# Kernel tuning notes

Hardware: AMD Instinct MI355X
Metric: run time of the kernel (lower is better)

## Reference

```python
import jax, jax.numpy as jnp
import numpy as np

D = 20          # embedding dim (hardcoded in original module)
N_REL = 200     # relation vocab size (table has N_REL+1 rows)
N_TIME = 365    # time embedding table size
L = 3           # propagation layers
E = 2_000_000   # edges per layer
N = 1_000_000   # node-slot pool per layer
B = 64          # batch size
N_ENT = 1_000_003


def setup_inputs() -> dict:
    key = jax.random.key(0)
    ks = jax.random.split(key, 16)
    src_idx = jax.random.randint(ks[0], (L, E), 0, N, dtype=jnp.int32)
    dst_idx = jax.random.randint(ks[1], (L, E), 0, N, dtype=jnp.int32)
    rel_idx = jax.random.randint(ks[2], (L, E), 0, N_REL + 1, dtype=jnp.int32)
    qrel_idx = jax.random.randint(ks[3], (L, E), 0, N_REL + 1, dtype=jnp.int32)
    # signed relative time (edge_time - query_time); abs() must stay < N_TIME
    rel_time = jax.random.randint(ks[4], (L, E), -(N_TIME - 1), N_TIME, dtype=jnp.int32)
    node_batch = jax.random.randint(ks[5], (N,), 0, B, dtype=jnp.int32)
    node_ent = jnp.arange(N, dtype=jnp.int32)  # unique entity per final node slot
    s = 0.1
    rela_embed = jax.random.normal(ks[6], (N_REL + 1, D), jnp.float32) * s
    time_embed = jax.random.normal(ks[7], (N_TIME, D), jnp.float32) * s
    w_att1 = jax.random.normal(ks[8], (30, 3 * D), jnp.float32) * s
    w_att2 = jax.random.normal(ks[9], (1, 30), jnp.float32) * s
    w_past = jax.random.normal(ks[10], (D, D), jnp.float32) * s
    w_now = jax.random.normal(ks[11], (D, D), jnp.float32) * s
    w_future = jax.random.normal(ks[12], (D, D), jnp.float32) * s
    w_cls = jax.random.normal(ks[13], (D,), jnp.float32) * s
    b_cls = jnp.zeros((), jnp.float32)
    return dict(src_idx=src_idx, dst_idx=dst_idx, rel_idx=rel_idx,
                qrel_idx=qrel_idx, rel_time=rel_time, node_batch=node_batch,
                node_ent=node_ent, rela_embed=rela_embed, time_embed=time_embed,
                w_att1=w_att1, w_att2=w_att2, w_past=w_past, w_now=w_now,
                w_future=w_future, w_cls=w_cls, b_cls=b_cls,
                batch_size=B, n_ent=N_ENT)


def reference(src_idx, dst_idx, rel_idx, qrel_idx, rel_time, node_batch,
              node_ent, rela_embed, time_embed, w_att1, w_att2, w_past,
              w_now, w_future, w_cls, b_cls, batch_size, n_ent):
    n_layers = src_idx.shape[0]
    n_nodes = node_batch.shape[0]
    d = rela_embed.shape[1]
    hidden = jnp.zeros((n_nodes, d), dtype=rela_embed.dtype)
    for l in range(n_layers):
        rt = rel_time[l]                         # [E] signed relative time
        h_src = hidden[src_idx[l]]               # [E, D] gather
        r_emb = rela_embed[rel_idx[l]]           # [E, D]
        t_emb = time_embed[jnp.abs(rt)]          # [E, D]
        embed_rel = h_src + r_emb + t_emb
        # conditional time-branch MLP (mask-partitioned linear, same math as
        # the original's boolean-masked assignments)
        fut = embed_rel @ w_future.T
        now = embed_rel @ w_now.T
        pst = embed_rel @ w_past.T
        transformed = jnp.where((rt > 0)[:, None], fut,
                       jnp.where((rt == 0)[:, None], now, pst))
        # attention over concat(hidden_src, rel_emb, query_rel_emb)  [E, 3D]
        att_in = jnp.concatenate([h_src, r_emb, rela_embed[qrel_idx[l]]], axis=1)
        score = jax.nn.sigmoid(jax.nn.relu(att_in @ w_att1.T) @ w_att2.T)  # [E,1]
        msg = score * transformed                # [E, D]
        hidden = jax.ops.segment_sum(msg, dst_idx[l], num_segments=n_nodes)
        hidden = jax.nn.leaky_relu(hidden)       # default slope 0.01, as torch
    result = hidden @ w_cls + b_cls              # [N]
    score_all = jnp.zeros((batch_size, n_ent), dtype=result.dtype)
    score_all = score_all.at[node_batch, node_ent].set(result)
    return score_all
```

## Files before the change

kernel.cpp:

```cpp
#include <hip/hip_runtime.h>
#include <hip/hip_bf16.h>
#include <cstdint>

#define DD 20
#define HID 30
#define NB_SCAN 1024
#define HROW 32

typedef unsigned int  u32;
typedef unsigned short u16;

__device__ __forceinline__ void load20(const float* __restrict__ p, float* r){
  const float4* q = (const float4*)p;
#pragma unroll
  for (int i=0;i<5;i++){ float4 v=q[i]; r[4*i+0]=v.x; r[4*i+1]=v.y; r[4*i+2]=v.z; r[4*i+3]=v.w; }
}

__device__ __forceinline__ u32 pkbf(float a, float b){
  u32 ua=__float_as_uint(a); ua=(ua+0x7FFFu+((ua>>16)&1u))>>16;
  u32 ub=__float_as_uint(b); ub=(ub+0x7FFFu+((ub>>16)&1u))>>16;
  return ua | (ub<<16);
}

__global__ void k_prep(const float* __restrict__ rela, const float* __restrict__ w1,
                       const float* __restrict__ wp, const float* __restrict__ wn,
                       const float* __restrict__ wf,
                       float* __restrict__ W3, float* __restrict__ AR, float* __restrict__ AQ,
                       int nrel){
  int t = blockIdx.x*blockDim.x + threadIdx.x;
  if (t < 3*DD*DD){
    int s = t/(DD*DD), idx = t%(DD*DD);
    W3[t] = (s==0)?wp[idx]:((s==1)?wn[idx]:wf[idx]);
  }
  if (t < nrel*HID){
    int r=t/HID, j=t-r*HID;
    float sr=0.f, sq=0.f;
#pragma unroll
    for (int k=0;k<DD;k++){
      float e = rela[r*DD+k];
      sr += e*w1[j*3*DD + DD + k];
      sq += e*w1[j*3*DD + 2*DD + k];
    }
    AR[r*32+j]=sr; AQ[r*32+j]=sq;
  }
}

__global__ void k_rwtw(const float* __restrict__ rela, const float* __restrict__ timee,
                       const float* __restrict__ W3,
                       float* __restrict__ RW, float* __restrict__ TW,
                       int nrel, int ntime){
  int t = blockIdx.x*blockDim.x+threadIdx.x;
  int totR = 3*nrel*DD, totT = 3*ntime*DD;
  if (t < totR){
    int sel = t/(nrel*DD); int rem = t - sel*nrel*DD; int r = rem/DD; int i = rem - r*DD;
    const float* w = W3 + sel*DD*DD + i*DD;
    const float* e = rela + (size_t)r*DD;
    float s=0.f;
#pragma unroll
    for (int k=0;k<DD;k++) s += e[k]*w[k];
    RW[t]=s;
  }
  if (t < totT){
    int sel = t/(ntime*DD); int rem = t - sel*ntime*DD; int tt = rem/DD; int i = rem - tt*DD;
    const float* w = W3 + sel*DD*DD + i*DD;
    const float* e = timee + (size_t)tt*DD;
    float s=0.f;
#pragma unroll
    for (int k=0;k<DD;k++) s += e[k]*w[k];
    TW[t]=s;
  }
}

__global__ void k_rt(const float* __restrict__ rela, const float* __restrict__ timee,
                     const float* __restrict__ W3, float* __restrict__ RT,
                     int nrel, int ntime){
  int row = blockIdx.x*blockDim.x+threadIdx.x;
  int tot = 3*nrel*ntime;
  if (row>=tot) return;
  int per = nrel*ntime;
  int sel = row/per; int rem = row - sel*per; int r = rem/ntime; int t = rem - r*ntime;
  float e[DD], tv[DD];
  load20(rela + (size_t)r*DD, e);
  load20(timee + (size_t)t*DD, tv);
#pragma unroll
  for (int k=0;k<DD;k++) e[k]+=tv[k];
  const float* W = W3 + sel*DD*DD;
  float o[DD];
#pragma unroll
  for (int i=0;i<DD;i++){
    const float4* wr = (const float4*)(W + i*DD);
    float s=0.f;
#pragma unroll
    for (int c=0;c<5;c++){ float4 w=wr[c]; s += e[4*c]*w.x + e[4*c+1]*w.y + e[4*c+2]*w.z + e[4*c+3]*w.w; }
    o[i]=s;
  }
  float4* op=(float4*)(RT + (size_t)row*DD);
#pragma unroll
  for (int c=0;c<5;c++){ float4 v; v.x=o[4*c]; v.y=o[4*c+1]; v.z=o[4*c+2]; v.w=o[4*c+3]; op[c]=v; }
}

__global__ void __launch_bounds__(256) k_pre(const int* __restrict__ dst, int* __restrict__ cnt,
        int* __restrict__ rank, int E, int N,
        float4* __restrict__ dout4, size_t nd4,
        uint4* __restrict__ b0, uint4* __restrict__ b1, size_t nbB4,
        float4* __restrict__ bF, size_t nf4,
        float4* __restrict__ res4, size_t nr4){
  int g=blockIdx.x, tid=threadIdx.x;
  int half=gridDim.x>>1;
  if (g & 1){
    int stride=half*256;
    int E2=2*E;
    for (int e=(g>>1)*256+tid; e<E2; e+=stride){
      int l=(e>=E)?1:0;
      rank[e]=atomicAdd(&cnt[(size_t)l*N+dst[e]],1);
    }
  } else {
    float4 z=make_float4(0.f,0.f,0.f,0.f);
    uint4 zu=make_uint4(0u,0u,0u,0u);
    size_t i=(size_t)(g>>1)*256+tid, st=(size_t)half*256;
    for (size_t k=i;k<nd4;k+=st) dout4[k]=z;
    for (size_t k=i;k<nbB4;k+=st){ b0[k]=zu; b1[k]=zu; }
    for (size_t k=i;k<nf4;k+=st) bF[k]=z;
    for (size_t k=i;k<nr4;k+=st) res4[k]=z;
  }
}

__global__ void k_scan_part(const int* __restrict__ cnt, int* __restrict__ part, int M, int C){
  __shared__ int sm[256];
  int b=blockIdx.x, t=threadIdx.x;
  int lo=b*C, hi=lo+C; if (hi>M) hi=M; if (lo>M) lo=M;
  int s=0;
  for (int i=lo+t; i<hi; i+=256) s+=cnt[i];
  sm[t]=s; __syncthreads();
  for (int o=128;o>0;o>>=1){ if (t<o) sm[t]+=sm[t+o]; __syncthreads(); }
  if (t==0) part[b]=sm[0];
}

__global__ void k_scan_top(int* __restrict__ part, int* __restrict__ listc){
  __shared__ int sm[NB_SCAN];
  int t=threadIdx.x;
  if (t==0) *listc=0;
  int v=part[t]; sm[t]=v; __syncthreads();
  for (int o=1;o<NB_SCAN;o<<=1){
    int u=(t>=o)?sm[t-o]:0; __syncthreads();
    sm[t]+=u; __syncthreads();
  }
  part[t]=sm[t]-v;
}

__global__ void k_scan_write(const int* __restrict__ cnt, const int* __restrict__ part,
                             int* __restrict__ rowptr, int M, int C){
  __shared__ int sm[256];
  int b=blockIdx.x, t=threadIdx.x;
  int lo=b*C, hi=lo+C; if (hi>M) hi=M; if (lo>M) lo=M;
  int run=part[b];
  for (int base=lo; base<hi; base+=256){
    int i=base+t;
    int v=(i<hi)?cnt[i]:0;
    sm[t]=v; __syncthreads();
    for (int o=1;o<256;o<<=1){
      int u=(t>=o)?sm[t-o]:0; __syncthreads();
      sm[t]+=u; __syncthreads();
    }
    if (i<hi) rowptr[i]=run+sm[t]-v;
    int tot=sm[255];
    __syncthreads();
    run+=tot;
  }
  if (hi==M && t==0) rowptr[M]=run;
}

__global__ void __launch_bounds__(256) k_scat(const int* __restrict__ src,const int* __restrict__ dst,
  const int* __restrict__ rel,const int* __restrict__ qrel,const int* __restrict__ rtm,
  const int* __restrict__ rank,const int* __restrict__ rowptr,int4* __restrict__ recs,int E){
  int e=blockIdx.x*blockDim.x+threadIdx.x;
  if (e>=E) return;
  int d=dst[e];
  int pos=rowptr[d]+rank[e];
  recs[pos]=make_int4(src[e], rel[e]|(qrel[e]<<16), rtm[e], d);
}

template<bool HASH,bool FINAL,int XR>
__global__ void __launch_bounds__(256) k_fused(
    const int4* __restrict__ recs,
    const u16* __restrict__ hin, u16* __restrict__ hout, float* __restrict__ bufF,
    const float* __restrict__ RW, const float* __restrict__ TW,
    const float* __restrict__ AR, const float* __restrict__ AQ,
    const float* __restrict__ w1, const float* __restrict__ w2, const float* __restrict__ W3,
    int E, int nrel, int ntime,
    const int* __restrict__ sA_src, const int* __restrict__ sA_dst,
    const int* __restrict__ sA_rel, const int* __restrict__ sA_qrel,
    const int* __restrict__ sA_rtm, const int* __restrict__ sA_rank,
    const int* __restrict__ sA_rowptr, int4* __restrict__ sA_recs, int sA_E,
    const int* __restrict__ hB_dst, int* __restrict__ hB_cnt, int* __restrict__ hB_rank, int hB_E,
    const float* __restrict__ wcls, float* __restrict__ res,
    int* __restrict__ list, int* __restrict__ listc)
{
  int g=blockIdx.x;
  if (XR>0){
    const int M=2+XR;
    int r=g%M, b=g/M, R=gridDim.x/M;
    if (r==2){
      int stride=R*256;
      for (int e=b*256+threadIdx.x; e<sA_E; e+=stride){
        int d=sA_dst[e];
        int pos=sA_rowptr[d]+sA_rank[e];
        sA_recs[pos]=make_int4(sA_src[e], sA_rel[e]|(sA_qrel[e]<<16), sA_rtm[e], d);
      }
      return;
    }
    if (XR>1 && r==3){
      int stride=R*256;
      for (int e=b*256+threadIdx.x; e<hB_E; e+=stride)
        hB_rank[e]=atomicAdd(&hB_cnt[hB_dst[e]],1);
      return;
    }
    g = b*2+r;
  }
  int bstart=g*256;
  if (bstart>=E) return;

  __shared__ float sW1h[HID*DD];
  __shared__ float sW2[32];
  __shared__ float sW3[3*DD*DD];
  __shared__ u32   smsg[256*10];
  __shared__ int   sdst[256];
  __shared__ int   s_prevdst, s_nextdst;
  if (HASH){
    for (int t=threadIdx.x; t<HID*DD; t+=blockDim.x){ int j=t/DD,k=t-j*DD; sW1h[t]=w1[j*3*DD+k]; }
    for (int t=threadIdx.x; t<3*DD*DD; t+=blockDim.x) sW3[t]=W3[t];
  }
  if (threadIdx.x<HID) sW2[threadIdx.x]=w2[threadIdx.x];

  int tid = threadIdx.x;
  int bsize = E - bstart; if (bsize>256) bsize=256;
  int j = bstart + tid;
  bool active = (tid < bsize);

  if (tid==0){
    s_prevdst = (bstart>0) ? recs[-1 + (ptrdiff_t)bstart].w : -1;
    s_nextdst = (bstart+bsize < E) ? recs[bstart+bsize].w : -1;
  }
  __syncthreads();

  int dstv = -1;
  float m[DD];
  if (active){
    int4 rc = recs[j];
    int s = rc.x;
    int r = rc.y & 0xFFFF;
    int q = ((unsigned)rc.y) >> 16;
    int t = rc.z;
    dstv  = rc.w;
    int sel = (t>0)?2:((t==0)?1:0);
    int ta = (t<0)?-t:t;

    float h[DD];
    if (HASH){
      const uint4* hp=(const uint4*)(hin+(size_t)s*HROW);
      uint4 A=hp[0], B=hp[1]; uint2 Cc=*((const uint2*)(hp+2));
      h[0]=__uint_as_float(A.x<<16);  h[1]=__uint_as_float(A.x&0xFFFF0000u);
      h[2]=__uint_as_float(A.y<<16);  h[3]=__uint_as_float(A.y&0xFFFF0000u);
      h[4]=__uint_as_float(A.z<<16);  h[5]=__uint_as_float(A.z&0xFFFF0000u);
      h[6]=__uint_as_float(A.w<<16);  h[7]=__uint_as_float(A.w&0xFFFF0000u);
      h[8]=__uint_as_float(B.x<<16);  h[9]=__uint_as_float(B.x&0xFFFF0000u);
      h[10]=__uint_as_float(B.y<<16); h[11]=__uint_as_float(B.y&0xFFFF0000u);
      h[12]=__uint_as_float(B.z<<16); h[13]=__uint_as_float(B.z&0xFFFF0000u);
      h[14]=__uint_as_float(B.w<<16); h[15]=__uint_as_float(B.w&0xFFFF0000u);
      h[16]=__uint_as_float(Cc.x<<16);h[17]=__uint_as_float(Cc.x&0xFFFF0000u);
      h[18]=__uint_as_float(Cc.y<<16);h[19]=__uint_as_float(Cc.y&0xFFFF0000u);
    }

    float z=0.f;
    {
      const float4* ap=(const float4*)(AR+(size_t)r*32);
      const float4* qp=(const float4*)(AQ+(size_t)q*32);
#pragma unroll
      for (int c=0;c<7;c++){
        float4 x=ap[c], y=qp[c];
        float s4[4]={x.x+y.x, x.y+y.y, x.z+y.z, x.w+y.w};
#pragma unroll
        for (int u=0;u<4;u++){
          int jj=4*c+u;
          if (HASH){
            const float4* wr=(const float4*)&sW1h[jj*DD];
            float sum=s4[u];
#pragma unroll
            for (int c2=0;c2<5;c2++){ float4 w=wr[c2]; sum += h[4*c2]*w.x+h[4*c2+1]*w.y+h[4*c2+2]*w.z+h[4*c2+3]*w.w; }
            s4[u]=sum;
          }
          z += fmaxf(s4[u],0.f)*sW2[jj];
        }
      }
      float2 x2=*(const float2*)(AR+(size_t)r*32+28);
      float2 y2=*(const float2*)(AQ+(size_t)q*32+28);
      float s0=x2.x+y2.x, s1=x2.y+y2.y;
      if (HASH){
        const float4* wr0=(const float4*)&sW1h[28*DD];
        const float4* wr1=(const float4*)&sW1h[29*DD];
#pragma unroll
        for (int c2=0;c2<5;c2++){
          float4 wA=wr0[c2], wB=wr1[c2];
          s0 += h[4*c2]*wA.x+h[4*c2+1]*wA.y+h[4*c2+2]*wA.z+h[4*c2+3]*wA.w;
          s1 += h[4*c2]*wB.x+h[4*c2+1]*wB.y+h[4*c2+2]*wB.z+h[4*c2+3]*wB.w;
        }
      }
      z += fmaxf(s0,0.f)*sW2[28] + fmaxf(s1,0.f)*sW2[29];
    }
    float score = 1.f/(1.f+__expf(-z));

    const float4* rwp=(const float4*)(RW + ((size_t)(sel*nrel+r))*DD);
    const float4* twp=(const float4*)(TW + ((size_t)(sel*ntime+ta))*DD);
#pragma unroll
    for (int c=0;c<5;c++){
      float4 a4=rwp[c], b4=twp[c];
      float mv[4]={a4.x+b4.x, a4.y+b4.y, a4.z+b4.z, a4.w+b4.w};
      if (HASH){
#pragma unroll
        for (int u=0;u<4;u++){
          const float4* wr=(const float4*)&sW3[sel*DD*DD+(4*c+u)*DD];
          float sum=mv[u];
#pragma unroll
          for (int c2=0;c2<5;c2++){ float4 w=wr[c2]; sum += h[4*c2]*w.x+h[4*c2+1]*w.y+h[4*c2+2]*w.z+h[4*c2+3]*w.w; }
          mv[u]=sum;
        }
      }
#pragma unroll
      for (int u=0;u<4;u++) m[4*c+u]=score*mv[u];
    }
#pragma unroll
    for (int i2=0;i2<10;i2++) smsg[tid*10+i2]=pkbf(m[2*i2],m[2*i2+1]);
  }
  sdst[tid] = active ? dstv : -2;
  __syncthreads();

  if (!active) return;
  bool isHead = (tid==0) ? (s_prevdst != dstv) : (sdst[tid-1] != dstv);
  if (!(isHead || tid==0)) return;
  int k=tid+1;
  for (; k<bsize && sdst[k]==dstv; ++k){
    const u32* row=&smsg[k*10];
#pragma unroll
    for (int i2=0;i2<10;i2++){
      u32 w=row[i2];
      m[2*i2]  +=__uint_as_float(w<<16);
      m[2*i2+1]+=__uint_as_float(w&0xFFFF0000u);
    }
  }
  bool crossStart = (tid==0 && !isHead);
  bool crossEnd   = (k==bsize) && (s_nextdst==dstv);
  if (crossStart || crossEnd){
    float* o = bufF + (size_t)dstv*DD;
#pragma unroll
    for (int i=0;i<DD;i++) atomicAdd(o+i, m[i]);
    if (!FINAL && isHead){
      int p = atomicAdd(listc,1);
      list[p] = dstv;
    }
  } else {
    if (!FINAL){
      u32 o10[10];
#pragma unroll
      for (int i2=0;i2<10;i2++){
        float x0=m[2*i2], x1=m[2*i2+1];
        x0=fmaxf(x0,0.01f*x0); x1=fmaxf(x1,0.01f*x1);
        o10[i2]=pkbf(x0,x1);
      }
      uint4* hp=(uint4*)(hout+(size_t)dstv*HROW);
      hp[0]=make_uint4(o10[0],o10[1],o10[2],o10[3]);
      hp[1]=make_uint4(o10[4],o10[5],o10[6],o10[7]);
      *((uint2*)(hp+2))=make_uint2(o10[8],o10[9]);
    } else {
      float rsum=0.f;
#pragma unroll
      for (int i=0;i<DD;i++){ float x=fmaxf(m[i],0.01f*m[i]); rsum += x*wcls[i]; }
      res[dstv] = rsum;
    }
  }
}

__global__ void __launch_bounds__(256) k_fixup(float* __restrict__ bufF, u16* __restrict__ hout,
   const int* __restrict__ list,const int* __restrict__ listc){
  int c=*listc;
  for (int i=blockIdx.x*blockDim.x+threadIdx.x; i<c; i+=gridDim.x*blockDim.x){
    int n=list[i];
    float* p=bufF+(size_t)n*DD;
    float v[DD];
#pragma unroll
    for (int jj=0;jj<DD;jj++){ v[jj]=p[jj]; p[jj]=0.f; }
    u32 o10[10];
#pragma unroll
    for (int i2=0;i2<10;i2++){
      float x0=v[2*i2], x1=v[2*i2+1];
      x0=fmaxf(x0,0.01f*x0); x1=fmaxf(x1,0.01f*x1);
      o10[i2]=pkbf(x0,x1);
    }
    uint4* hp=(uint4*)(hout+(size_t)n*HROW);
    hp[0]=make_uint4(o10[0],o10[1],o10[2],o10[3]);
    hp[1]=make_uint4(o10[4],o10[5],o10[6],o10[7]);
    *((uint2*)(hp+2))=make_uint2(o10[8],o10[9]);
  }
}

__global__ void __launch_bounds__(256) k_out(const float* __restrict__ res,
   const float* __restrict__ bufF, const float* __restrict__ wcls, const float* __restrict__ bcls,
   const int* __restrict__ nb, const int* __restrict__ ne, const int* __restrict__ nentp,
   float* __restrict__ out, int N){
  int n=blockIdx.x*blockDim.x+threadIdx.x;
  if (n>=N) return;
  float acc = res[n] + bcls[0];
  const float4* q=(const float4*)(bufF+(size_t)n*DD);
#pragma unroll
  for (int c=0;c<5;c++){
    float4 v=q[c];
    acc += fmaxf(v.x,0.01f*v.x)*wcls[4*c]   + fmaxf(v.y,0.01f*v.y)*wcls[4*c+1]
         + fmaxf(v.z,0.01f*v.z)*wcls[4*c+2] + fmaxf(v.w,0.01f*v.w)*wcls[4*c+3];
  }
  long long stride = nentp[0];
  out[(long long)nb[n]*stride + ne[n]] = acc;
}

template<bool HASH>
__global__ void __launch_bounds__(256) k_edge(
    const int* __restrict__ src, const int* __restrict__ dst,
    const int* __restrict__ rel, const int* __restrict__ qrel,
    const int* __restrict__ rtm,
    const float* __restrict__ hin, float* __restrict__ hout,
    const float* __restrict__ RT, const float* __restrict__ AR, const float* __restrict__ AQ,
    const float* __restrict__ w1, const float* __restrict__ w2, const float* __restrict__ W3,
    int E, int nrel, int ntime)
{
  __shared__ float sW1h[HID*DD];
  __shared__ float sW2[32];
  __shared__ float sW3[3*DD*DD];
  for (int t=threadIdx.x; t<HID*DD; t+=blockDim.x){ int j=t/DD,k=t-j*DD; sW1h[t]=w1[j*3*DD+k]; }
  if (threadIdx.x<HID) sW2[threadIdx.x]=w2[threadIdx.x];
  for (int t=threadIdx.x; t<3*DD*DD; t+=blockDim.x) sW3[t]=W3[t];
  __syncthreads();
  int e = blockIdx.x*blockDim.x+threadIdx.x;
  if (e>=E) return;
  int s=src[e], d=dst[e], r=rel[e], q=qrel[e], t=rtm[e];
  int sel = (t>0)?2:((t==0)?1:0);
  int ta = (t<0)?-t:t;
  float h[DD];
  if (HASH){
    load20(hin+(size_t)s*DD, h);
#pragma unroll
    for (int i=0;i<DD;i++) h[i]=fmaxf(h[i],0.01f*h[i]);
  }
  float a[HID];
  {
    const float4* ap=(const float4*)(AR+(size_t)r*32);
    const float4* qp=(const float4*)(AQ+(size_t)q*32);
#pragma unroll
    for (int c=0;c<7;c++){
      float4 x=ap[c], y=qp[c];
      a[4*c+0]=x.x+y.x; a[4*c+1]=x.y+y.y; a[4*c+2]=x.z+y.z; a[4*c+3]=x.w+y.w;
    }
    float2 x=*(const float2*)(AR+(size_t)r*32+28);
    float2 y=*(const float2*)(AQ+(size_t)q*32+28);
    a[28]=x.x+y.x; a[29]=x.y+y.y;
  }
  if (HASH){
#pragma unroll
    for (int j=0;j<HID;j++){
      const float4* wr=(const float4*)&sW1h[j*DD];
      float sum=a[j];
#pragma unroll
      for (int c=0;c<5;c++){ float4 w=wr[c]; sum += h[4*c]*w.x+h[4*c+1]*w.y+h[4*c+2]*w.z+h[4*c+3]*w.w; }
      a[j]=sum;
    }
  }
  float z=0.f;
#pragma unroll
  for (int j=0;j<HID;j++) z += fmaxf(a[j],0.f)*sW2[j];
  float score = 1.f/(1.f+__expf(-z));
  float tr[DD];
  load20(RT + ((size_t)(sel*nrel+r)*ntime + ta)*DD, tr);
  if (HASH){
    const float* Ws = sW3 + sel*DD*DD;
#pragma unroll
    for (int i=0;i<DD;i++){
      const float4* wr=(const float4*)(Ws+i*DD);
      float sum=tr[i];
#pragma unroll
      for (int c=0;c<5;c++){ float4 w=wr[c]; sum += h[4*c]*w.x+h[4*c+1]*w.y+h[4*c+2]*w.z+h[4*c+3]*w.w; }
      tr[i]=sum;
    }
  }
  float* o = hout + (size_t)d*DD;
#pragma unroll
  for (int i=0;i<DD;i++) atomicAdd(o+i, score*tr[i]);
}

__global__ void k_result(const float* __restrict__ h, const float* __restrict__ wcls,
                         const float* __restrict__ bcls, float* __restrict__ res, int N){
  int i = blockIdx.x*blockDim.x+threadIdx.x;
  if (i>=N) return;
  float acc = bcls[0];
  const float4* q=(const float4*)(h+(size_t)i*DD);
#pragma unroll
  for (int c=0;c<5;c++){
    float4 v=q[c];
    float x0=fmaxf(v.x,0.01f*v.x), x1=fmaxf(v.y,0.01f*v.y);
    float x2=fmaxf(v.z,0.01f*v.z), x3=fmaxf(v.w,0.01f*v.w);
    acc += x0*wcls[4*c]+x1*wcls[4*c+1]+x2*wcls[4*c+2]+x3*wcls[4*c+3];
  }
  res[i]=acc;
}

__global__ void k_scatter(const float* __restrict__ res, const int* __restrict__ nb,
                          const int* __restrict__ ne, const int* __restrict__ nentp,
                          float* __restrict__ out, int N){
  int i=blockIdx.x*blockDim.x+threadIdx.x;
  if (i>=N) return;
  long long stride = nentp[0];
  out[(long long)nb[i]*stride + ne[i]] = res[i];
}

extern "C" void kernel_launch(void* const* d_in, const int* in_sizes, int n_in,
                              void* d_out, int out_size, void* d_ws, size_t ws_size,
                              hipStream_t stream){
  const int*   src =(const int*)d_in[0];
  const int*   dst =(const int*)d_in[1];
  const int*   rel =(const int*)d_in[2];
  const int*   qrel=(const int*)d_in[3];
  const int*   rtm =(const int*)d_in[4];
  const int*   nb  =(const int*)d_in[5];
  const int*   ne  =(const int*)d_in[6];
  const float* rela=(const float*)d_in[7];
  const float* timee=(const float*)d_in[8];
  const float* w1  =(const float*)d_in[9];
  const float* w2  =(const float*)d_in[10];
  const float* wp  =(const float*)d_in[11];
  const float* wn  =(const float*)d_in[12];
  const float* wf  =(const float*)d_in[13];
  const float* wcls=(const float*)d_in[14];
  const float* bcls=(const float*)d_in[15];
  const int*   nentp=(const int*)d_in[17];

  const int Lc=3;
  int LE=in_sizes[0]; int E=LE/Lc;
  int N=in_sizes[5];
  int nrel=in_sizes[7]/DD;
  int ntime=in_sizes[8]/DD;

  auto al=[](size_t x){ return (x+(size_t)255)&~(size_t)255; };
  size_t szBufB=al((size_t)N*HROW*2);
  size_t szBufF=al((size_t)N*DD*4);
  size_t szBuf =al((size_t)N*DD*4);
  size_t szRW  =al((size_t)3*nrel*DD*4);
  size_t szTW  =al((size_t)3*ntime*DD*4);
  size_t szRTf =al((size_t)3*nrel*ntime*DD*4);
  size_t szA   =al((size_t)nrel*32*4);
  size_t szW3  =al((size_t)3*DD*DD*4);
  size_t szRow =al((size_t)Lc*((size_t)N+1)*4);
  size_t szRank=al((size_t)LE*4);
  size_t szCnt =al((size_t)Lc*N*4);
  size_t szRecs=al((size_t)LE*16);
  size_t szPart=al((size_t)NB_SCAN*4);
  size_t szList=al((size_t)(131072+16)*4);
  size_t szRes =al((size_t)N*4);
  size_t need = 2*szBufB+szBufF+szRW+szTW+2*szA+szW3+szRow+szRank+szCnt+szRecs+szPart+szList+szRes;

  dim3 blk(256);
  int prepTot = (3*DD*DD > nrel*HID) ? 3*DD*DD : nrel*HID;
  int rtTot=3*nrel*ntime;
  int rwtwTot = 3*ntime*DD;

  if (ws_size >= need){
    char* base=(char*)d_ws;
    size_t off=0;
    u16*   b0 =(u16*)(base+off);   off+=szBufB;
    u16*   b1 =(u16*)(base+off);   off+=szBufB;
    float* bufF=(float*)(base+off); off+=szBufF;
    float* RW  =(float*)(base+off); off+=szRW;
    float* TW  =(float*)(base+off); off+=szTW;
    float* AR  =(float*)(base+off); off+=szA;
    float* AQ  =(float*)(base+off); off+=szA;
    float* W3  =(float*)(base+off); off+=szW3;
    int*   rowptr=(int*)(base+off); off+=szRow;
    int*   rank=(int*)(base+off);  off+=szRank;
    int*   cnt =(int*)(base+off);  off+=szCnt;
    int4*  recs=(int4*)(base+off); off+=szRecs;
    int*   part=(int*)(base+off);  off+=szPart;
    int*   listc=(int*)(base+off);
    int*   list =listc+16;          off+=szList;
    float* res =(float*)(base+off); off+=szRes;

    float* dout=(float*)d_out;

    (void)hipMemsetAsync(cnt,0,(size_t)Lc*N*4,stream);
    k_prep<<<dim3((prepTot+255)/256),blk,0,stream>>>(rela,w1,wp,wn,wf,W3,AR,AQ,nrel);
    k_rwtw<<<dim3((rwtwTot+255)/256),blk,0,stream>>>(rela,timee,W3,RW,TW,nrel,ntime);

    size_t nd4=(size_t)out_size>>2;
    size_t nbB4=(size_t)N*HROW*2/16;
    size_t nf4=(size_t)N*DD/4;
    size_t nr4=(size_t)N/4;
    k_pre<<<dim3(8192),blk,0,stream>>>(dst,cnt,rank,E,N,(float4*)dout,nd4,
                                       (uint4*)b0,(uint4*)b1,nbB4,(float4*)bufF,nf4,
                                       (float4*)res,nr4);

    int C=(N+NB_SCAN-1)/NB_SCAN;
    int LB=(E+255)/256;
    int H=(LB+1)/2;

    for (int l=0;l<2;++l){
      int* cnt_l = cnt + (size_t)l*N;
      int* row_l = rowptr + (size_t)l*(N+1);
      k_scan_part<<<dim3(NB_SCAN),blk,0,stream>>>(cnt_l,part,N,C);
      k_scan_top<<<dim3(1),dim3(NB_SCAN),0,stream>>>(part,listc);
      k_scan_write<<<dim3(NB_SCAN),blk,0,stream>>>(cnt_l,part,row_l,N,C);
    }
    k_scat<<<dim3(LB),blk,0,stream>>>(src,dst,rel,qrel,rtm,rank,rowptr,recs,E);

    k_fused<false,false,2><<<dim3(4*H),blk,0,stream>>>(recs,nullptr,b0,bufF,
        RW,TW,AR,AQ,w1,w2,W3,E,nrel,ntime,
        src+(size_t)E,dst+(size_t)E,rel+(size_t)E,qrel+(size_t)E,rtm+(size_t)E,
        rank+(size_t)E,rowptr+(size_t)(N+1),recs+(size_t)E,E,
        dst+(size_t)2*E,cnt+(size_t)2*N,rank+(size_t)2*E,E,
        wcls,res,list,listc);
    k_fixup<<<dim3(128),blk,0,stream>>>(bufF,b0,list,listc);

    {
      int* cnt_l = cnt + (size_t)2*N;
      int* row_l = rowptr + (size_t)2*(N+1);
      k_scan_part<<<dim3(NB_SCAN),blk,0,stream>>>(cnt_l,part,N,C);
      k_scan_top<<<dim3(1),dim3(NB_SCAN),0,stream>>>(part,listc);
      k_scan_write<<<dim3(NB_SCAN),blk,0,stream>>>(cnt_l,part,row_l,N,C);
    }

    k_fused<true,false,1><<<dim3(3*H),blk,0,stream>>>(recs+(size_t)E,b0,b1,bufF,
        RW,TW,AR,AQ,w1,w2,W3,E,nrel,ntime,
        src+(size_t)2*E,dst+(size_t)2*E,rel+(size_t)2*E,qrel+(size_t)2*E,rtm+(size_t)2*E,
        rank+(size_t)2*E,rowptr+(size_t)2*(N+1),recs+(size_t)2*E,E,
        nullptr,nullptr,nullptr,0,
        wcls,res,list,listc);
    k_fixup<<<dim3(128),blk,0,stream>>>(bufF,b1,list,listc);

    k_fused<true,true,0><<<dim3(LB),blk,0,stream>>>(recs+(size_t)2*E,b1,nullptr,bufF,
        RW,TW,AR,AQ,w1,w2,W3,E,nrel,ntime,
        nullptr,nullptr,nullptr,nullptr,nullptr,nullptr,nullptr,nullptr,0,
        nullptr,nullptr,nullptr,0,
        wcls,res,list,listc);

    k_out<<<dim3((N+255)/256),blk,0,stream>>>(res,bufF,wcls,bcls,nb,ne,nentp,dout,N);
  } else {
    char* base=(char*)d_out; float* res=(float*)d_ws;
    size_t off=0;
    float* buf0=(float*)(base+off); off+=szBuf;
    float* buf1=(float*)(base+off); off+=szBuf;
    float* RT  =(float*)(base+off); off+=szRTf;
    float* AR  =(float*)(base+off); off+=szA;
    float* AQ  =(float*)(base+off); off+=szA;
    float* W3  =(float*)(base+off); off+=szW3;
    k_prep<<<dim3((prepTot+255)/256),blk,0,stream>>>(rela,w1,wp,wn,wf,W3,AR,AQ,nrel);
    k_rt<<<dim3((rtTot+255)/256),blk,0,stream>>>(rela,timee,W3,RT,nrel,ntime);
    dim3 egrid((E+255)/256);
    dim3 ngrid((N+255)/256);
    (void)hipMemsetAsync(buf0,0,(size_t)N*DD*4,stream);
    k_edge<false><<<egrid,blk,0,stream>>>(src,dst,rel,qrel,rtm,nullptr,buf0,RT,AR,AQ,w1,w2,W3,E,nrel,ntime);
    (void)hipMemsetAsync(buf1,0,(size_t)N*DD*4,stream);
    k_edge<true><<<egrid,blk,0,stream>>>(src+(size_t)E,dst+(size_t)E,rel+(size_t)E,qrel+(size_t)E,rtm+(size_t)E,
                                         buf0,buf1,RT,AR,AQ,w1,w2,W3,E,nrel,ntime);
    (void)hipMemsetAsync(buf0,0,(size_t)N*DD*4,stream);
    k_edge<true><<<egrid,blk,0,stream>>>(src+(size_t)2*E,dst+(size_t)2*E,rel+(size_t)2*E,qrel+(size_t)2*E,rtm+(size_t)2*E,
                                         buf1,buf0,RT,AR,AQ,w1,w2,W3,E,nrel,ntime);
    k_result<<<ngrid,blk,0,stream>>>(buf0,wcls,bcls,res,N);
    (void)hipMemsetAsync(d_out,0,(size_t)out_size*sizeof(float),stream);
    k_scatter<<<ngrid,blk,0,stream>>>(res,nb,ne,nentp,(float*)d_out,N);
  }
}
```

Baseline: 1.102 ms.

## Store hidden states in fp32 and merge layer 0/1 scans and scatters

Replaces the bf16 packed hidden-state buffers (32-element padded rows) with plain fp32 20-float rows. Leaky ReLU now runs on the consumer side, and shared-memory message staging uses fp32 with a padded row stride of 21. The layer-0 and layer-1 prefix scans and record scatters are merged into one scan over 2N counts and one scatter kernel. Layer-2's scatter moves out of the fused layer-1 kernel into its own launch. This cuts launch count and pack/unpack ALU work, but each hidden-state gather row grows from 64 to 80 bytes and the shared-memory footprint rises.

Measured after the change: 1.053 ms. -4.4%, faster.

```diff
diff --git a/kernel.cpp b/kernel.cpp
--- a/kernel.cpp
+++ b/kernel.cpp
@@ -5,7 +5,7 @@
 #define DD 20
 #define HID 30
 #define NB_SCAN 1024
-#define HROW 32
+#define MROW 21
 
 typedef unsigned int  u32;
 typedef unsigned short u16;
@@ -14,12 +14,6 @@
   const float4* q = (const float4*)p;
 #pragma unroll
   for (int i=0;i<5;i++){ float4 v=q[i]; r[4*i+0]=v.x; r[4*i+1]=v.y; r[4*i+2]=v.z; r[4*i+3]=v.w; }
-}
-
-__device__ __forceinline__ u32 pkbf(float a, float b){
-  u32 ua=__float_as_uint(a); ua=(ua+0x7FFFu+((ua>>16)&1u))>>16;
-  u32 ub=__float_as_uint(b); ub=(ub+0x7FFFu+((ub>>16)&1u))>>16;
-  return ua | (ub<<16);
 }
 
 __global__ void k_prep(const float* __restrict__ rela, const float* __restrict__ w1,
@@ -102,7 +96,7 @@
 __global__ void __launch_bounds__(256) k_pre(const int* __restrict__ dst, int* __restrict__ cnt,
         int* __restrict__ rank, int E, int N,
         float4* __restrict__ dout4, size_t nd4,
-        uint4* __restrict__ b0, uint4* __restrict__ b1, size_t nbB4,
+        float4* __restrict__ b0, float4* __restrict__ b1, size_t nb4,
         float4* __restrict__ bF, size_t nf4,
         float4* __restrict__ res4, size_t nr4){
   int g=blockIdx.x, tid=threadIdx.x;
@@ -116,10 +110,9 @@
     }
   } else {
     float4 z=make_float4(0.f,0.f,0.f,0.f);
-    uint4 zu=make_uint4(0u,0u,0u,0u);
     size_t i=(size_t)(g>>1)*256+tid, st=(size_t)half*256;
     for (size_t k=i;k<nd4;k+=st) dout4[k]=z;
-    for (size_t k=i;k<nbB4;k+=st){ b0[k]=zu; b1[k]=zu; }
+    for (size_t k=i;k<nb4;k+=st){ b0[k]=z; b1[k]=z; }
     for (size_t k=i;k<nf4;k+=st) bF[k]=z;
     for (size_t k=i;k<nr4;k+=st) res4[k]=z;
   }
@@ -149,13 +142,13 @@
 }
 
 __global__ void k_scan_write(const int* __restrict__ cnt, const int* __restrict__ part,
-                             int* __restrict__ rowptr, int M, int C){
+                             int* __restrict__ rowptr, int M, int C, int base){
   __shared__ int sm[256];
   int b=blockIdx.x, t=threadIdx.x;
   int lo=b*C, hi=lo+C; if (hi>M) hi=M; if (lo>M) lo=M;
-  int run=part[b];
-  for (int base=lo; base<hi; base+=256){
-    int i=base+t;
+  int run=part[b]+base;
+  for (int bb=lo; bb<hi; bb+=256){
+    int i=bb+t;
     int v=(i<hi)?cnt[i]:0;
     sm[t]=v; __syncthreads();
     for (int o=1;o<256;o<<=1){
@@ -170,60 +163,59 @@
   if (hi==M && t==0) rowptr[M]=run;
 }
 
-__global__ void __launch_bounds__(256) k_scat(const int* __restrict__ src,const int* __restrict__ dst,
+__global__ void __launch_bounds__(256) k_scat01(const int* __restrict__ src,const int* __restrict__ dst,
   const int* __restrict__ rel,const int* __restrict__ qrel,const int* __restrict__ rtm,
-  const int* __restrict__ rank,const int* __restrict__ rowptr,int4* __restrict__ recs,int E){
+  const int* __restrict__ rank,const int* __restrict__ rowptr,int4* __restrict__ recs,int E,int N){
+  int e=blockIdx.x*blockDim.x+threadIdx.x;
+  if (e>=2*E) return;
+  int l=(e>=E)?1:0;
+  int d=dst[e];
+  int pos=rowptr[(size_t)l*N+d]+rank[e];
+  recs[pos]=make_int4(src[e], rel[e]|(qrel[e]<<16), rtm[e], d);
+}
+
+__global__ void __launch_bounds__(256) k_scat2(const int* __restrict__ src,const int* __restrict__ dst,
+  const int* __restrict__ rel,const int* __restrict__ qrel,const int* __restrict__ rtm,
+  const int* __restrict__ rank,const int* __restrict__ rowptr2,int4* __restrict__ recs,int E){
   int e=blockIdx.x*blockDim.x+threadIdx.x;
   if (e>=E) return;
   int d=dst[e];
-  int pos=rowptr[d]+rank[e];
+  int pos=rowptr2[d]+rank[e];
   recs[pos]=make_int4(src[e], rel[e]|(qrel[e]<<16), rtm[e], d);
 }
 
-template<bool HASH,bool FINAL,int XR>
+template<bool HASH,bool FINAL,bool HIST>
 __global__ void __launch_bounds__(256) k_fused(
     const int4* __restrict__ recs,
-    const u16* __restrict__ hin, u16* __restrict__ hout, float* __restrict__ bufF,
+    const float* __restrict__ hin, float* __restrict__ hout, float* __restrict__ bufF,
     const float* __restrict__ RW, const float* __restrict__ TW,
     const float* __restrict__ AR, const float* __restrict__ AQ,
     const float* __restrict__ w1, const float* __restrict__ w2, const float* __restrict__ W3,
     int E, int nrel, int ntime,
-    const int* __restrict__ sA_src, const int* __restrict__ sA_dst,
-    const int* __restrict__ sA_rel, const int* __restrict__ sA_qrel,
-    const int* __restrict__ sA_rtm, const int* __restrict__ sA_rank,
-    const int* __restrict__ sA_rowptr, int4* __restrict__ sA_recs, int sA_E,
     const int* __restrict__ hB_dst, int* __restrict__ hB_cnt, int* __restrict__ hB_rank, int hB_E,
     const float* __restrict__ wcls, float* __restrict__ res,
     int* __restrict__ list, int* __restrict__ listc)
 {
-  int g=blockIdx.x;
-  if (XR>0){
-    const int M=2+XR;
-    int r=g%M, b=g/M, R=gridDim.x/M;
-    if (r==2){
-      int stride=R*256;
-      for (int e=b*256+threadIdx.x; e<sA_E; e+=stride){
-        int d=sA_dst[e];
-        int pos=sA_rowptr[d]+sA_rank[e];
-        sA_recs[pos]=make_int4(sA_src[e], sA_rel[e]|(sA_qrel[e]<<16), sA_rtm[e], d);
-      }
-      return;
-    }
-    if (XR>1 && r==3){
-      int stride=R*256;
-      for (int e=b*256+threadIdx.x; e<hB_E; e+=stride)
+  int lb;
+  if (HIST){
+    int g=blockIdx.x;
+    int r3=g%3, b3=g/3;
+    if (r3==2){
+      int H=gridDim.x/3;
+      int stride=H*256;
+      for (int e=b3*256+threadIdx.x; e<hB_E; e+=stride)
         hB_rank[e]=atomicAdd(&hB_cnt[hB_dst[e]],1);
       return;
     }
-    g = b*2+r;
-  }
-  int bstart=g*256;
+    lb=b3*2+r3;
+  } else lb=blockIdx.x;
+  int bstart=lb*256;
   if (bstart>=E) return;
 
   __shared__ float sW1h[HID*DD];
   __shared__ float sW2[32];
   __shared__ float sW3[3*DD*DD];
-  __shared__ u32   smsg[256*10];
+  __shared__ float smsg[256*MROW];
   __shared__ int   sdst[256];
   __shared__ int   s_prevdst, s_nextdst;
   if (HASH){
@@ -257,18 +249,9 @@
 
     float h[DD];
     if (HASH){
-      const uint4* hp=(const uint4*)(hin+(size_t)s*HROW);
-      uint4 A=hp[0], B=hp[1]; uint2 Cc=*((const uint2*)(hp+2));
-      h[0]=__uint_as_float(A.x<<16);  h[1]=__uint_as_float(A.x&0xFFFF0000u);
-      h[2]=__uint_as_float(A.y<<16);  h[3]=__uint_as_float(A.y&0xFFFF0000u);
-      h[4]=__uint_as_float(A.z<<16);  h[5]=__uint_as_float(A.z&0xFFFF0000u);
-      h[6]=__uint_as_float(A.w<<16);  h[7]=__uint_as_float(A.w&0xFFFF0000u);
-      h[8]=__uint_as_float(B.x<<16);  h[9]=__uint_as_float(B.x&0xFFFF0000u);
-      h[10]=__uint_as_float(B.y<<16); h[11]=__uint_as_float(B.y&0xFFFF0000u);
-      h[12]=__uint_as_float(B.z<<16); h[13]=__uint_as_float(B.z&0xFFFF0000u);
-      h[14]=__uint_as_float(B.w<<16); h[15]=__uint_as_float(B.w&0xFFFF0000u);
-      h[16]=__uint_as_float(Cc.x<<16);h[17]=__uint_as_float(Cc.x&0xFFFF0000u);
-      h[18]=__uint_as_float(Cc.y<<16);h[19]=__uint_as_float(Cc.y&0xFFFF0000u);
+      load20(hin+(size_t)s*DD, h);
+#pragma unroll
+      for (int i=0;i<DD;i++) h[i]=fmaxf(h[i],0.01f*h[i]);
     }
 
     float z=0.f;
@@ -326,10 +309,8 @@
         }
       }
 #pragma unroll
-      for (int u=0;u<4;u++) m[4*c+u]=score*mv[u];
-    }
-#pragma unroll
-    for (int i2=0;i2<10;i2++) smsg[tid*10+i2]=pkbf(m[2*i2],m[2*i2+1]);
+      for (int u=0;u<4;u++){ m[4*c+u]=score*mv[u]; smsg[tid*MROW+4*c+u]=m[4*c+u]; }
+    }
   }
   sdst[tid] = active ? dstv : -2;
   __syncthreads();
@@ -339,13 +320,9 @@
   if (!(isHead || tid==0)) return;
   int k=tid+1;
   for (; k<bsize && sdst[k]==dstv; ++k){
-    const u32* row=&smsg[k*10];
-#pragma unroll
-    for (int i2=0;i2<10;i2++){
-      u32 w=row[i2];
-      m[2*i2]  +=__uint_as_float(w<<16);
-      m[2*i2+1]+=__uint_as_float(w&0xFFFF0000u);
-    }
+    const float* row=&smsg[k*MROW];
+#pragma unroll
+    for (int i=0;i<DD;i++) m[i]+=row[i];
   }
   bool crossStart = (tid==0 && !isHead);
   bool crossEnd   = (k==bsize) && (s_nextdst==dstv);
@@ -359,17 +336,9 @@
     }
   } else {
     if (!FINAL){
-      u32 o10[10];
-#pragma unroll
-      for (int i2=0;i2<10;i2++){
-        float x0=m[2*i2], x1=m[2*i2+1];
-        x0=fmaxf(x0,0.01f*x0); x1=fmaxf(x1,0.01f*x1);
-        o10[i2]=pkbf(x0,x1);
-      }
-      uint4* hp=(uint4*)(hout+(size_t)dstv*HROW);
-      hp[0]=make_uint4(o10[0],o10[1],o10[2],o10[3]);
-      hp[1]=make_uint4(o10[4],o10[5],o10[6],o10[7]);
-      *((uint2*)(hp+2))=make_uint2(o10[8],o10[9]);
+      float4* op=(float4*)(hout + (size_t)dstv*DD);
+#pragma unroll
+      for (int c=0;c<5;c++){ float4 v; v.x=m[4*c]; v.y=m[4*c+1]; v.z=m[4*c+2]; v.w=m[4*c+3]; op[c]=v; }
     } else {
       float rsum=0.f;
 #pragma unroll
@@ -379,26 +348,15 @@
   }
 }
 
-__global__ void __launch_bounds__(256) k_fixup(float* __restrict__ bufF, u16* __restrict__ hout,
+__global__ void __launch_bounds__(256) k_fixup(float* __restrict__ bufF, float* __restrict__ hout,
    const int* __restrict__ list,const int* __restrict__ listc){
   int c=*listc;
   for (int i=blockIdx.x*blockDim.x+threadIdx.x; i<c; i+=gridDim.x*blockDim.x){
     int n=list[i];
     float* p=bufF+(size_t)n*DD;
-    float v[DD];
-#pragma unroll
-    for (int jj=0;jj<DD;jj++){ v[jj]=p[jj]; p[jj]=0.f; }
-    u32 o10[10];
-#pragma unroll
-    for (int i2=0;i2<10;i2++){
-      float x0=v[2*i2], x1=v[2*i2+1];
-      x0=fmaxf(x0,0.01f*x0); x1=fmaxf(x1,0.01f*x1);
-      o10[i2]=pkbf(x0,x1);
-    }
-    uint4* hp=(uint4*)(hout+(size_t)n*HROW);
-    hp[0]=make_uint4(o10[0],o10[1],o10[2],o10[3]);
-    hp[1]=make_uint4(o10[4],o10[5],o10[6],o10[7]);
-    *((uint2*)(hp+2))=make_uint2(o10[8],o10[9]);
+    float* o=hout+(size_t)n*DD;
+#pragma unroll
+    for (int jj=0;jj<DD;jj++){ o[jj]=p[jj]; p[jj]=0.f; }
   }
 }
 
@@ -546,22 +504,20 @@
   int ntime=in_sizes[8]/DD;
 
   auto al=[](size_t x){ return (x+(size_t)255)&~(size_t)255; };
-  size_t szBufB=al((size_t)N*HROW*2);
-  size_t szBufF=al((size_t)N*DD*4);
   size_t szBuf =al((size_t)N*DD*4);
   size_t szRW  =al((size_t)3*nrel*DD*4);
   size_t szTW  =al((size_t)3*ntime*DD*4);
   size_t szRTf =al((size_t)3*nrel*ntime*DD*4);
   size_t szA   =al((size_t)nrel*32*4);
   size_t szW3  =al((size_t)3*DD*DD*4);
-  size_t szRow =al((size_t)Lc*((size_t)N+1)*4);
+  size_t szRow =al(((size_t)3*N+3)*4);
   size_t szRank=al((size_t)LE*4);
   size_t szCnt =al((size_t)Lc*N*4);
   size_t szRecs=al((size_t)LE*16);
   size_t szPart=al((size_t)NB_SCAN*4);
   size_t szList=al((size_t)(131072+16)*4);
   size_t szRes =al((size_t)N*4);
-  size_t need = 2*szBufB+szBufF+szRW+szTW+2*szA+szW3+szRow+szRank+szCnt+szRecs+szPart+szList+szRes;
+  size_t need = 3*szBuf+szRW+szTW+2*szA+szW3+szRow+szRank+szCnt+szRecs+szPart+szList+szRes;
 
   dim3 blk(256);
   int prepTot = (3*DD*DD > nrel*HID) ? 3*DD*DD : nrel*HID;
@@ -571,15 +527,16 @@
   if (ws_size >= need){
     char* base=(char*)d_ws;
     size_t off=0;
-    u16*   b0 =(u16*)(base+off);   off+=szBufB;
-    u16*   b1 =(u16*)(base+off);   off+=szBufB;
-    float* bufF=(float*)(base+off); off+=szBufF;
+    float* b0 =(float*)(base+off);  off+=szBuf;
+    float* b1 =(float*)(base+off);  off+=szBuf;
+    float* bufF=(float*)(base+off); off+=szBuf;
     float* RW  =(float*)(base+off); off+=szRW;
     float* TW  =(float*)(base+off); off+=szTW;
     float* AR  =(float*)(base+off); off+=szA;
     float* AQ  =(float*)(base+off); off+=szA;
     float* W3  =(float*)(base+off); off+=szW3;
     int*   rowptr=(int*)(base+off); off+=szRow;
+    int*   rowptr2=rowptr+(size_t)2*N+1;
     int*   rank=(int*)(base+off);  off+=szRank;
     int*   cnt =(int*)(base+off);  off+=szCnt;
     int4*  recs=(int4*)(base+off); off+=szRecs;
@@ -595,53 +552,46 @@
     k_rwtw<<<dim3((rwtwTot+255)/256),blk,0,stream>>>(rela,timee,W3,RW,TW,nrel,ntime);
 
     size_t nd4=(size_t)out_size>>2;
-    size_t nbB4=(size_t)N*HROW*2/16;
-    size_t nf4=(size_t)N*DD/4;
+    size_t nb4=(size_t)N*DD/4;
     size_t nr4=(size_t)N/4;
     k_pre<<<dim3(8192),blk,0,stream>>>(dst,cnt,rank,E,N,(float4*)dout,nd4,
-                                       (uint4*)b0,(uint4*)b1,nbB4,(float4*)bufF,nf4,
+                                       (float4*)b0,(float4*)b1,nb4,(float4*)bufF,nb4,
                                        (float4*)res,nr4);
 
-    int C=(N+NB_SCAN-1)/NB_SCAN;
     int LB=(E+255)/256;
     int H=(LB+1)/2;
 
-    for (int l=0;l<2;++l){
-      int* cnt_l = cnt + (size_t)l*N;
-      int* row_l = rowptr + (size_t)l*(N+1);
-      k_scan_part<<<dim3(NB_SCAN),blk,0,stream>>>(cnt_l,part,N,C);
+    {
+      int M=2*N, C=(M+NB_SCAN-1)/NB_SCAN;
+      k_scan_part<<<dim3(NB_SCAN),blk,0,stream>>>(cnt,part,M,C);
       k_scan_top<<<dim3(1),dim3(NB_SCAN),0,stream>>>(part,listc);
-      k_scan_write<<<dim3(NB_SCAN),blk,0,stream>>>(cnt_l,part,row_l,N,C);
-    }
-    k_scat<<<dim3(LB),blk,0,stream>>>(src,dst,rel,qrel,rtm,rank,rowptr,recs,E);
-
-    k_fused<false,false,2><<<dim3(4*H),blk,0,stream>>>(recs,nullptr,b0,bufF,
+      k_scan_write<<<dim3(NB_SCAN),blk,0,stream>>>(cnt,part,rowptr,M,C,0);
+    }
+    k_scat01<<<dim3((2*E+255)/256),blk,0,stream>>>(src,dst,rel,qrel,rtm,rank,rowptr,recs,E,N);
+
+    k_fused<false,false,true><<<dim3(3*H),blk,0,stream>>>(recs,nullptr,b0,bufF,
         RW,TW,AR,AQ,w1,w2,W3,E,nrel,ntime,
-        src+(size_t)E,dst+(size_t)E,rel+(size_t)E,qrel+(size_t)E,rtm+(size_t)E,
-        rank+(size_t)E,rowptr+(size_t)(N+1),recs+(size_t)E,E,
         dst+(size_t)2*E,cnt+(size_t)2*N,rank+(size_t)2*E,E,
         wcls,res,list,listc);
     k_fixup<<<dim3(128),blk,0,stream>>>(bufF,b0,list,listc);
 
     {
-      int* cnt_l = cnt + (size_t)2*N;
-      int* row_l = rowptr + (size_t)2*(N+1);
-      k_scan_part<<<dim3(NB_SCAN),blk,0,stream>>>(cnt_l,part,N,C);
+      int C=(N+NB_SCAN-1)/NB_SCAN;
+      k_scan_part<<<dim3(NB_SCAN),blk,0,stream>>>(cnt+(size_t)2*N,part,N,C);
       k_scan_top<<<dim3(1),dim3(NB_SCAN),0,stream>>>(part,listc);
-      k_scan_write<<<dim3(NB_SCAN),blk,0,stream>>>(cnt_l,part,row_l,N,C);
-    }
-
-    k_fused<true,false,1><<<dim3(3*H),blk,0,stream>>>(recs+(size_t)E,b0,b1,bufF,
+      k_scan_write<<<dim3(NB_SCAN),blk,0,stream>>>(cnt+(size_t)2*N,part,rowptr2,N,C,2*E);
+    }
+    k_scat2<<<dim3(LB),blk,0,stream>>>(src+(size_t)2*E,dst+(size_t)2*E,rel+(size_t)2*E,
+        qrel+(size_t)2*E,rtm+(size_t)2*E,rank+(size_t)2*E,rowptr2,recs,E);
+
+    k_fused<true,false,false><<<dim3(LB),blk,0,stream>>>(recs+(size_t)E,b0,b1,bufF,
         RW,TW,AR,AQ,w1,w2,W3,E,nrel,ntime,
-        src+(size_t)2*E,dst+(size_t)2*E,rel+(size_t)2*E,qrel+(size_t)2*E,rtm+(size_t)2*E,
-        rank+(size_t)2*E,rowptr+(size_t)2*(N+1),recs+(size_t)2*E,E,
         nullptr,nullptr,nullptr,0,
         wcls,res,list,listc);
     k_fixup<<<dim3(128),blk,0,stream>>>(bufF,b1,list,listc);
 
-    k_fused<true,true,0><<<dim3(LB),blk,0,stream>>>(recs+(size_t)2*E,b1,nullptr,bufF,
+    k_fused<true,true,false><<<dim3(LB),blk,0,stream>>>(recs+(size_t)2*E,b1,nullptr,bufF,
         RW,TW,AR,AQ,w1,w2,W3,E,nrel,ntime,
-        nullptr,nullptr,nullptr,nullptr,nullptr,nullptr,nullptr,nullptr,0,
         nullptr,nullptr,nullptr,0,
         wcls,res,list,listc);
 
```
